# Optimization experiments

Hardware: AMD Instinct MI355X
Metric: run time of the kernel (lower is better)

## Reference

```python
import jax, jax.numpy as jnp
import numpy as np
from jax import lax

N, C1, C2, H, W = 4, 256, 256, 80, 80
CH = 128           # c_ = int(c2 * e)
G, KS = 1, 3       # groups, kernel_size
K = KS * KS        # sampling points per group
PAD, DIL = 1, 1
EPS_BN, EPS_LN = 1e-5, 1e-6


def conv_bn_silu(x, w, g, b, m, v, stride=1):
    # ultralytics Conv: conv(bias=False) + BatchNorm2d(eval) + SiLU
    pad = (w.shape[2] - 1) // 2
    y = lax.conv_general_dilated(x, w, (stride, stride), [(pad, pad), (pad, pad)],
                                 dimension_numbers=('NCHW', 'OIHW', 'NCHW'))
    s = g / jnp.sqrt(v + EPS_BN)
    y = y * s[None, :, None, None] + (b - m * s)[None, :, None, None]
    return jax.nn.silu(y)


def dcnv3_core(x, offset, mask):
    # x: (N,H,W,C) NHWC; offset: (N,H,W,G*K*2); mask: (N,H,W,G,K) softmaxed over K
    n, h, w, c = x.shape
    gc = c // G
    xp = jnp.pad(x, ((0, 0), (PAD, PAD), (PAD, PAD), (0, 0)))
    Hp, Wp = h + 2 * PAD, w + 2 * PAD
    base = (DIL * (KS - 1)) // 2
    # reference points (normalized by padded spatial size), stride 1
    ref_x = (jnp.arange(w, dtype=x.dtype) + base + 0.5) / Wp   # (W,)
    ref_y = (jnp.arange(h, dtype=x.dtype) + base + 0.5) / Hp   # (H,)
    gx = (jnp.arange(KS, dtype=x.dtype) * DIL - base) / Wp
    gy = (jnp.arange(KS, dtype=x.dtype) * DIL - base) / Hp
    grid_x = jnp.repeat(gx, KS)   # point p = i*KS + j -> x = gx[i]
    grid_y = jnp.tile(gy, KS)     # y = gy[j]  (torch meshgrid 'ij' ordering)
    off = offset.reshape(n, h, w, G, K, 2)
    loc_x = ref_x[None, None, :, None, None] + grid_x + off[..., 0] / Wp
    loc_y = ref_y[None, :, None, None, None] + grid_y + off[..., 1] / Hp
    # grid_sample align_corners=False: pixel = norm * size - 0.5
    px = loc_x * Wp - 0.5
    py = loc_y * Hp - 0.5
    x0 = jnp.floor(px); y0 = jnp.floor(py)
    lw, lh = px - x0, py - y0
    x0i, y0i = x0.astype(jnp.int32), y0.astype(jnp.int32)
    xv = jnp.transpose(xp.reshape(n, Hp * Wp, G, gc), (0, 2, 1, 3))  # (N,G,S,gc)
    tw = lambda a: jnp.transpose(a, (0, 3, 1, 2, 4))[..., None]      # (N,H,W,G,K)->(N,G,H,W,K,1)

    def gather(yi, xi):
        valid = ((xi >= 0) & (xi < Wp) & (yi >= 0) & (yi < Hp)).astype(x.dtype)
        idx = jnp.clip(yi, 0, Hp - 1) * Wp + jnp.clip(xi, 0, Wp - 1)
        idx = jnp.transpose(idx, (0, 3, 1, 2, 4)).reshape(n, G, h * w * K)
        v = jnp.take_along_axis(xv, idx[..., None], axis=2).reshape(n, G, h, w, K, gc)
        return v * tw(valid)   # zeros padding_mode

    out = (gather(y0i, x0i) * tw((1 - lh) * (1 - lw))
           + gather(y0i, x0i + 1) * tw((1 - lh) * lw)
           + gather(y0i + 1, x0i) * tw(lh * (1 - lw))
           + gather(y0i + 1, x0i + 1) * tw(lh * lw))   # (N,G,H,W,K,gc)
    m = jnp.transpose(mask, (0, 3, 1, 2, 4))[..., None]
    out = (out * m).sum(axis=4)                        # (N,G,H,W,gc)
    return jnp.transpose(out, (0, 2, 3, 1, 4)).reshape(n, h, w, c)


def forward(x, w1, g1, b1, m1, v1, w2, g2, b2, m2, v2,
            dw_w, dw_b, ln_g, ln_b, off_w, off_b, msk_w, msk_b,
            in_w, in_b, out_w, out_b, g3, b3, m3, v3):
    y = conv_bn_silu(x, w1, g1, b1, m1, v1)   # cv1: 3x3 Conv c1->c_
    y = conv_bn_silu(y, w2, g2, b2, m2, v2)   # cv2.conv: 1x1 Conv c_->c2
    t = jnp.transpose(y, (0, 2, 3, 1))        # NHWC
    x_proj = t @ in_w.T + in_b                # input_proj
    # dw_conv: depthwise 3x3 -> LayerNorm (channels_last) -> GELU
    dw = lax.conv_general_dilated(y, dw_w, (1, 1), [(1, 1), (1, 1)],
                                  dimension_numbers=('NCHW', 'OIHW', 'NCHW'),
                                  feature_group_count=C2)
    dw = jnp.transpose(dw, (0, 2, 3, 1)) + dw_b
    mu = dw.mean(-1, keepdims=True)
    var = ((dw - mu) ** 2).mean(-1, keepdims=True)
    dw = (dw - mu) / jnp.sqrt(var + EPS_LN) * ln_g + ln_b
    dw = jax.nn.gelu(dw, approximate=False)
    offset = dw @ off_w.T + off_b                                       # (N,H,W,G*K*2)
    mask = jax.nn.softmax((dw @ msk_w.T + msk_b).reshape(N, H, W, G, K), axis=-1)
    z = dcnv3_core(x_proj, offset, mask)
    z = z @ out_w.T + out_b                   # output_proj
    z = jnp.transpose(z, (0, 3, 1, 2))        # NCHW
    s = g3 / jnp.sqrt(v3 + EPS_BN)
    z = z * s[None, :, None, None] + (b3 - m3 * s)[None, :, None, None]
    z = jax.nn.silu(z)
    return x + z                              # shortcut (c1 == c2)


def setup_inputs():
    key = jax.random.key(0)
    ks = jax.random.split(key, 16)
    r = lambda k, s, sc=0.05: jax.random.normal(k, s, dtype=jnp.float32) * sc
    return {
        'x': jax.random.normal(ks[0], (N, C1, H, W), dtype=jnp.float32),
        'w1': r(ks[1], (CH, C1, 3, 3)),
        'g1': jnp.ones((CH,), jnp.float32), 'b1': jnp.zeros((CH,), jnp.float32),
        'm1': r(ks[2], (CH,), 0.1),
        'v1': jax.random.uniform(ks[3], (CH,), jnp.float32, 0.5, 1.5),
        'w2': r(ks[4], (C2, CH, 1, 1)),
        'g2': jnp.ones((C2,), jnp.float32), 'b2': jnp.zeros((C2,), jnp.float32),
        'm2': r(ks[5], (C2,), 0.1),
        'v2': jax.random.uniform(ks[6], (C2,), jnp.float32, 0.5, 1.5),
        'dw_w': r(ks[7], (C2, 1, 3, 3)), 'dw_b': jnp.zeros((C2,), jnp.float32),
        'ln_g': jnp.ones((C2,), jnp.float32), 'ln_b': jnp.zeros((C2,), jnp.float32),
        'off_w': r(ks[8], (G * K * 2, C2), 0.01), 'off_b': jnp.zeros((G * K * 2,), jnp.float32),
        'msk_w': r(ks[9], (G * K, C2), 0.01), 'msk_b': jnp.zeros((G * K,), jnp.float32),
        'in_w': r(ks[10], (C2, C2)), 'in_b': jnp.zeros((C2,), jnp.float32),
        'out_w': r(ks[11], (C2, C2)), 'out_b': jnp.zeros((C2,), jnp.float32),
        'g3': jnp.ones((C2,), jnp.float32), 'b3': jnp.zeros((C2,), jnp.float32),
        'm3': r(ks[12], (C2,), 0.1),
        'v3': jax.random.uniform(ks[13], (C2,), jnp.float32, 0.5, 1.5),
    }


def reference(x, w1, g1, b1, m1, v1, w2, g2, b2, m2, v2,
              dw_w, dw_b, ln_g, ln_b, off_w, off_b, msk_w, msk_b,
              in_w, in_b, out_w, out_b, g3, b3, m3, v3):
    return forward(x, w1, g1, b1, m1, v1, w2, g2, b2, m2, v2,
                   dw_w, dw_b, ln_g, ln_b, off_w, off_b, msk_w, msk_b,
                   in_w, in_b, out_w, out_b, g3, b3, m3, v3)
```

## Files before the change

### kernel.cpp

```cpp
#include <hip/hip_runtime.h>
#include <cmath>

#define TN 4
#define TC1 256
#define TCH 128
#define TC2 256
#define TH 80
#define TW 80
#define THP 82
#define TWP 84
#define NPIX (TN*TH*TW)

#define OFF_WBF   0
#define OFF_W2B   294912
#define OFF_INWB  327680
#define OFF_OUTWB 393216
#define OFF_DWT   458752
#define OFF_WCAT  461056
#define OFF_WCATB 467968
#define OFF_T1    468128
#define OFF_T2    468512
#define OFF_T3P   469024
#define OFF_XPAD  469504
#define OFF_Y1B   3997696
#define OFF_Y2N   7525888
#define OFF_DWN   469504
#define OFF_RAWN  10802688
#define OFF_ZN    11493888

typedef __attribute__((ext_vector_type(8))) short bf16x8;
typedef __attribute__((ext_vector_type(4))) float f32x4;

__device__ __forceinline__ float siluf(float v) { return v / (1.f + expf(-v)); }
__device__ __forceinline__ short rnbf(float f) {
  unsigned u = __float_as_uint(f);
  unsigned r = (u + 0x7fffu + ((u >> 16) & 1u)) >> 16;
  return (short)r;
}
__device__ __forceinline__ float bf2f(short s) {
  return __uint_as_float(((unsigned)(unsigned short)s) << 16);
}

__global__ __launch_bounds__(256) void k_prep(
    const float* __restrict__ w1, const float* __restrict__ g1, const float* __restrict__ b1,
    const float* __restrict__ m1, const float* __restrict__ v1,
    const float* __restrict__ w2, const float* __restrict__ g2, const float* __restrict__ b2,
    const float* __restrict__ m2, const float* __restrict__ v2,
    const float* __restrict__ dww, const float* __restrict__ offw, const float* __restrict__ offb,
    const float* __restrict__ mskw, const float* __restrict__ mskb,
    const float* __restrict__ inw, const float* __restrict__ outw, const float* __restrict__ outb,
    const float* __restrict__ g3, const float* __restrict__ b3,
    const float* __restrict__ m3, const float* __restrict__ v3,
    float* __restrict__ ws)
{
  int i = blockIdx.x * 256 + threadIdx.x;
  if (i < 294912) {
    int co = i / 2304; int r = i - co * 2304;
    int tap = r >> 8; int ci = r & 255; int ky = tap / 3; int kx = tap - ky * 3;
    float s = g1[co] * __frsqrt_rn(v1[co] + 1e-5f);
    ((short*)(ws + OFF_WBF))[i] = rnbf(w1[((co * TC1 + ci) * 3 + ky) * 3 + kx] * s);
    return;
  }
  i -= 294912;
  if (i < 32768) {
    int co = i >> 7; int ci = i & 127;
    float s = g2[co] * __frsqrt_rn(v2[co] + 1e-5f);
    ((short*)(ws + OFF_W2B))[i] = rnbf(w2[co * TCH + ci] * s);
    return;
  }
  i -= 32768;
  if (i < 65536) {
    int co = i >> 8; int ci = i & 255;
    ((short*)(ws + OFF_INWB))[i] = rnbf(inw[co * TC2 + ci]);
    return;
  }
  i -= 65536;
  if (i < 65536) {
    int co = i >> 8; int ci = i & 255;
    float s = g3[co] * __frsqrt_rn(v3[co] + 1e-5f);
    ((short*)(ws + OFF_OUTWB))[i] = rnbf(outw[co * TC2 + ci] * s);
    return;
  }
  i -= 65536;
  if (i < 2304) { int c = i & 255; int j = i >> 8; ws[OFF_DWT + i] = dww[c * 9 + j]; return; }
  i -= 2304;
  if (i < 8192) {
    int c = i & 255; int j = i >> 8;
    float v = 0.f;
    if (j < 18) v = offw[j * 256 + c];
    else if (j < 27) v = mskw[(j - 18) * 256 + c];
    ((short*)(ws + OFF_WCAT))[i] = rnbf(v);
    return;
  }
  i -= 8192;
  if (i < 27) { ws[OFF_WCATB + i] = (i < 18) ? offb[i] : mskb[i - 18]; return; }
  i -= 27;
  if (i < 128) { float s = g1[i] / sqrtf(v1[i] + 1e-5f); ws[OFF_T1 + i] = b1[i] - m1[i] * s; return; }
  i -= 128;
  if (i < 256) { float s = g2[i] / sqrtf(v2[i] + 1e-5f); ws[OFF_T2 + i] = b2[i] - m2[i] * s; return; }
  i -= 256;
  if (i < 256) { float s = g3[i] / sqrtf(v3[i] + 1e-5f); ws[OFF_T3P + i] = outb[i] * s + b3[i] - m3[i] * s; return; }
}

__global__ __launch_bounds__(256) void k_padx(const float* __restrict__ x, short* __restrict__ xpn)
{
  __shared__ short lds[80 * 40];
  int b = blockIdx.x;
  int cc = b & 7; int hp = (b >> 3) % THP; int n = b / (THP * 8);
  int c0 = cc * 32;
  int t = threadIdx.x;
  int h = hp - 1;
  bool hv = (h >= 0 && h < TH);
  if (hv) {
    for (int f = t; f < 640; f += 256) {
      int ci = f / 20; int w4 = (f - ci * 20) * 4;
      float4 xv = *(const float4*)(x + ((n * TC1 + c0 + ci) * TH + h) * TW + w4);
      lds[(w4 + 0) * 40 + ci] = rnbf(xv.x);
      lds[(w4 + 1) * 40 + ci] = rnbf(xv.y);
      lds[(w4 + 2) * 40 + ci] = rnbf(xv.z);
      lds[(w4 + 3) * 40 + ci] = rnbf(xv.w);
    }
  }
  __syncthreads();
  short* op = xpn + ((n * THP + hp) * TWP) * TC2 + c0;
  for (int g = t; g < 672; g += 256) {
    int ci4 = (g & 7) * 4; int wp = g >> 3;
    short4 v = {0, 0, 0, 0};
    if (hv && wp >= 1 && wp <= TW) v = *(const short4*)(&lds[(wp - 1) * 40 + ci4]);
    *(short4*)(op + wp * TC2 + ci4) = v;
  }
}

#define BH_STR 40
#define BH_PIX 108
__global__ __launch_bounds__(256) void k_cv1f(const short* __restrict__ xpn, const short* __restrict__ wbf,
                                              const float* __restrict__ t1v, short* __restrict__ y1b)
{
  __shared__ short Bh[2][BH_PIX * BH_STR];

  int b = blockIdx.x;
  int wt = b % 5; b /= 5; int ht = b % 20; int n = b / 20;
  int w0 = wt * 16, h0 = ht * 4;

  int tid = threadIdx.x;
  int wave = tid >> 6, lane = tid & 63;
  int ln = lane & 15, q = lane >> 4;
  int co0 = wave * 32;

  int u0 = tid, u1 = tid + 256;
  int p0 = u0 >> 2, s0 = u0 & 3;
  int p1 = u1 >> 2, s1 = u1 & 3;
  int hh0 = p0 / 18, ww0 = p0 - hh0 * 18;
  int hh1 = p1 / 18, ww1 = p1 - hh1 * 18;
  const short* sb0 = xpn + ((n * THP + h0 + hh0) * TWP + (w0 + ww0)) * 256 + s0 * 8;
  const short* sb1 = xpn + ((n * THP + h0 + hh1) * TWP + (w0 + ww1)) * 256 + s1 * 8;
  bool hasu1 = (u1 < 432);
  int d0 = p0 * BH_STR + s0 * 8;
  int d1 = p1 * BH_STR + s1 * 8;

  const short* abase = wbf + (co0 + ln) * 2304 + q * 8;

  f32x4 acc[2][4];
#pragma unroll
  for (int i = 0; i < 2; ++i)
#pragma unroll
    for (int j = 0; j < 4; ++j) acc[i][j] = (f32x4){0.f, 0.f, 0.f, 0.f};

  bf16x8 rb0 = *(const bf16x8*)(sb0);
  bf16x8 rb1 = {0, 0, 0, 0, 0, 0, 0, 0};
  if (hasu1) rb1 = *(const bf16x8*)(sb1);
  *(bf16x8*)(&Bh[0][d0]) = rb0;
  if (hasu1) *(bf16x8*)(&Bh[0][d1]) = rb1;
  __syncthreads();

  for (int cc = 0; cc < 8; ++cc) {
    int cur = cc & 1;
    bf16x8 af[9][2];
#pragma unroll
    for (int tap = 0; tap < 9; ++tap)
#pragma unroll
      for (int mt = 0; mt < 2; ++mt)
        af[tap][mt] = *(const bf16x8*)(abase + (mt * 16) * 2304 + tap * 256 + cc * 32);
    if (cc < 7) {
      rb0 = *(const bf16x8*)(sb0 + (cc + 1) * 32);
      if (hasu1) rb1 = *(const bf16x8*)(sb1 + (cc + 1) * 32);
    }
#pragma unroll
    for (int tap = 0; tap < 9; ++tap) {
      const int ky = tap / 3, kx = tap - (tap / 3) * 3;
      bf16x8 bv[4];
#pragma unroll
      for (int nt = 0; nt < 4; ++nt) {
        int pr = nt * 16 + ln;
        int hr = pr >> 4, wc = pr & 15;
        bv[nt] = *(const bf16x8*)(&Bh[cur][((hr + ky) * 18 + (wc + kx)) * BH_STR + q * 8]);
      }
#pragma unroll
      for (int mt = 0; mt < 2; ++mt)
#pragma unroll
        for (int nt = 0; nt < 4; ++nt)
          acc[mt][nt] = __builtin_amdgcn_mfma_f32_16x16x32_bf16(af[tap][mt], bv[nt], acc[mt][nt], 0, 0, 0);
    }
    if (cc < 7) {
      *(bf16x8*)(&Bh[cur ^ 1][d0]) = rb0;
      if (hasu1) *(bf16x8*)(&Bh[cur ^ 1][d1]) = rb1;
      __syncthreads();
    }
  }

#pragma unroll
  for (int mt = 0; mt < 2; ++mt) {
    int co = co0 + mt * 16 + q * 4;
    float t0 = t1v[co], t1 = t1v[co + 1], t2 = t1v[co + 2], t3 = t1v[co + 3];
#pragma unroll
    for (int nt = 0; nt < 4; ++nt) {
      int pr = nt * 16 + ln;
      int hr = pr >> 4, wc = pr & 15;
      int pix = (n * TH + h0 + hr) * TW + (w0 + wc);
      short4 p;
      p.x = rnbf(siluf(acc[mt][nt][0] + t0));
      p.y = rnbf(siluf(acc[mt][nt][1] + t1));
      p.z = rnbf(siluf(acc[mt][nt][2] + t2));
      p.w = rnbf(siluf(acc[mt][nt][3] + t3));
      *(short4*)(y1b + pix * TCH + co) = p;
    }
  }
}

#define A_STR 40
__global__ __launch_bounds__(256) void k_cv2(const short* __restrict__ y1b, const short* __restrict__ w2b,
                                             const float* __restrict__ t2v, short* __restrict__ y2b)
{
  __shared__ short As[2][128 * A_STR];
  __shared__ short Bs[2][128 * A_STR];

  int b = blockIdx.x;
  int ch = b & 1; int pt = b >> 1;
  int co_base = ch * 128;
  int pix0 = pt * 128;

  int tid = threadIdx.x;
  int wave = tid >> 6, lane = tid & 63;
  int ln = lane & 15, q = lane >> 4;
  int coh = (wave & 1) * 64;
  int pxh = (wave >> 1) * 64;

  int srow = tid >> 1;
  int ssub = (tid & 1) * 16;
  const short* arow = w2b + (co_base + srow) * TCH + ssub;
  const short* brow = y1b + (pix0 + srow) * TCH + ssub;

  f32x4 acc[4][4];
#pragma unroll
  for (int i = 0; i < 4; ++i)
#pragma unroll
    for (int j = 0; j < 4; ++j) acc[i][j] = (f32x4){0.f, 0.f, 0.f, 0.f};

  bf16x8 ra0, ra1, rb0, rb1;
  auto grab = [&](int c) {
    const short* ap = arow + c * 32;
    const short* bp = brow + c * 32;
    ra0 = *(const bf16x8*)(ap);
    ra1 = *(const bf16x8*)(ap + 8);
    rb0 = *(const bf16x8*)(bp);
    rb1 = *(const bf16x8*)(bp + 8);
  };
  auto put = [&](int buf) {
    int o = srow * A_STR + ssub;
    *(bf16x8*)(&As[buf][o])     = ra0;
    *(bf16x8*)(&As[buf][o + 8]) = ra1;
    *(bf16x8*)(&Bs[buf][o])     = rb0;
    *(bf16x8*)(&Bs[buf][o + 8]) = rb1;
  };
  auto comp = [&](int buf) {
    bf16x8 af[4], bfv[4];
#pragma unroll
    for (int mt = 0; mt < 4; ++mt)
      af[mt] = *(const bf16x8*)(&As[buf][(coh + mt * 16 + ln) * A_STR + q * 8]);
#pragma unroll
    for (int nt = 0; nt < 4; ++nt)
      bfv[nt] = *(const bf16x8*)(&Bs[buf][(pxh + nt * 16 + ln) * A_STR + q * 8]);
#pragma unroll
    for (int mt = 0; mt < 4; ++mt)
#pragma unroll
      for (int nt = 0; nt < 4; ++nt)
        acc[mt][nt] = __builtin_amdgcn_mfma_f32_16x16x32_bf16(af[mt], bfv[nt], acc[mt][nt], 0, 0, 0);
  };

  const int NCH = TCH / 32;
  grab(0);
  put(0);
  __syncthreads();
  for (int c = 0; c < NCH; ++c) {
    if (c < NCH - 1) grab(c + 1);
    comp(c & 1);
    if (c < NCH - 1) {
      __syncthreads();
      put((c + 1) & 1);
      __syncthreads();
    }
  }

#pragma unroll
  for (int mt = 0; mt < 4; ++mt) {
    int co = co_base + coh + mt * 16 + q * 4;
    float t0 = t2v[co], t1 = t2v[co + 1], t2 = t2v[co + 2], t3 = t2v[co + 3];
#pragma unroll
    for (int nt = 0; nt < 4; ++nt) {
      int pix = pix0 + pxh + nt * 16 + ln;
      short4 p;
      p.x = rnbf(siluf(acc[mt][nt][0] + t0));
      p.y = rnbf(siluf(acc[mt][nt][1] + t1));
      p.z = rnbf(siluf(acc[mt][nt][2] + t2));
      p.w = rnbf(siluf(acc[mt][nt][3] + t3));
      *(short4*)(y2b + pix * TC2 + co) = p;
    }
  }
}

__global__ __launch_bounds__(256) void k_proj_in(const short* __restrict__ y2b, const short* __restrict__ inwb,
                                                 const float* __restrict__ inb, short* __restrict__ xproj)
{
  __shared__ short As[2][128 * A_STR];
  __shared__ short Bs[2][128 * A_STR];

  int b = blockIdx.x;
  int ch = b & 1; int pt = b >> 1;
  int co_base = ch * 128;
  int pix0 = pt * 128;

  int tid = threadIdx.x;
  int wave = tid >> 6, lane = tid & 63;
  int ln = lane & 15, q = lane >> 4;
  int coh = (wave & 1) * 64;
  int pxh = (wave >> 1) * 64;

  int srow = tid >> 1;
  int ssub = (tid & 1) * 16;
  const short* arow = inwb + (co_base + srow) * TC2 + ssub;
  const short* brow = y2b + (pix0 + srow) * TC2 + ssub;

  f32x4 acc[4][4];
#pragma unroll
  for (int i = 0; i < 4; ++i)
#pragma unroll
    for (int j = 0; j < 4; ++j) acc[i][j] = (f32x4){0.f, 0.f, 0.f, 0.f};

  bf16x8 ra0, ra1, rb0, rb1;
  auto grab = [&](int c) {
    const short* ap = arow + c * 32;
    const short* bp = brow + c * 32;
    ra0 = *(const bf16x8*)(ap);
    ra1 = *(const bf16x8*)(ap + 8);
    rb0 = *(const bf16x8*)(bp);
    rb1 = *(const bf16x8*)(bp + 8);
  };
  auto put = [&](int buf) {
    int o = srow * A_STR + ssub;
    *(bf16x8*)(&As[buf][o])     = ra0;
    *(bf16x8*)(&As[buf][o + 8]) = ra1;
    *(bf16x8*)(&Bs[buf][o])     = rb0;
    *(bf16x8*)(&Bs[buf][o + 8]) = rb1;
  };
  auto comp = [&](int buf) {
    bf16x8 af[4], bfv[4];
#pragma unroll
    for (int mt = 0; mt < 4; ++mt)
      af[mt] = *(const bf16x8*)(&As[buf][(coh + mt * 16 + ln) * A_STR + q * 8]);
#pragma unroll
    for (int nt = 0; nt < 4; ++nt)
      bfv[nt] = *(const bf16x8*)(&Bs[buf][(pxh + nt * 16 + ln) * A_STR + q * 8]);
#pragma unroll
    for (int mt = 0; mt < 4; ++mt)
#pragma unroll
      for (int nt = 0; nt < 4; ++nt)
        acc[mt][nt] = __builtin_amdgcn_mfma_f32_16x16x32_bf16(af[mt], bfv[nt], acc[mt][nt], 0, 0, 0);
  };

  const int NCH = TC2 / 32;
  grab(0);
  put(0);
  __syncthreads();
  for (int c = 0; c < NCH; ++c) {
    if (c < NCH - 1) grab(c + 1);
    comp(c & 1);
    if (c < NCH - 1) {
      __syncthreads();
      put((c + 1) & 1);
      __syncthreads();
    }
  }

#pragma unroll
  for (int mt = 0; mt < 4; ++mt) {
    int co = co_base + coh + mt * 16 + q * 4;
    float b0 = inb[co], b1 = inb[co + 1], b2 = inb[co + 2], b3 = inb[co + 3];
#pragma unroll
    for (int nt = 0; nt < 4; ++nt) {
      int pix = pix0 + pxh + nt * 16 + ln;
      short4 p;
      p.x = rnbf(acc[mt][nt][0] + b0);
      p.y = rnbf(acc[mt][nt][1] + b1);
      p.z = rnbf(acc[mt][nt][2] + b2);
      p.w = rnbf(acc[mt][nt][3] + b3);
      *(short4*)(xproj + pix * TC2 + co) = p;
    }
  }
}

__global__ __launch_bounds__(256) void k_dwln(const short* __restrict__ y2b, const float* __restrict__ dwt,
                                              const float* __restrict__ dwb, const float* __restrict__ lng,
                                              const float* __restrict__ lnb, short* __restrict__ dwo)
{
  int tid = threadIdx.x;
  int wave = tid >> 6, lane = tid & 63;
  int half = lane >> 5;
  int pix = blockIdx.x * 8 + wave * 2 + half;
  int w = pix % TW; int h = (pix / TW) % TH; int n = pix / (TH * TW);
  int c0 = (lane & 31) * 8;

  float v[8];
  {
    float4 b0 = *(const float4*)(dwb + c0);
    float4 b1 = *(const float4*)(dwb + c0 + 4);
    v[0] = b0.x; v[1] = b0.y; v[2] = b0.z; v[3] = b0.w;
    v[4] = b1.x; v[5] = b1.y; v[6] = b1.z; v[7] = b1.w;
  }
#pragma unroll
  for (int dy = 0; dy < 3; ++dy) {
#pragma unroll
    for (int dx = 0; dx < 3; ++dx) {
      int hh = h + dy - 1, ww = w + dx - 1;
      bool ok = (hh >= 0) & (hh < TH) & (ww >= 0) & (ww < TW);
      int off = ok ? (((n * TH + hh) * TW + ww) * TC2 + c0) : c0;
      bf16x8 yv = *(const bf16x8*)(y2b + off);
      float m = ok ? 1.f : 0.f;
      const float* wp = dwt + (dy * 3 + dx) * TC2 + c0;
      float4 w0 = *(const float4*)(wp);
      float4 w1 = *(const float4*)(wp + 4);
      v[0] += bf2f(yv[0]) * w0.x * m;
      v[1] += bf2f(yv[1]) * w0.y * m;
      v[2] += bf2f(yv[2]) * w0.z * m;
      v[3] += bf2f(yv[3]) * w0.w * m;
      v[4] += bf2f(yv[4]) * w1.x * m;
      v[5] += bf2f(yv[5]) * w1.y * m;
      v[6] += bf2f(yv[6]) * w1.z * m;
      v[7] += bf2f(yv[7]) * w1.w * m;
    }
  }
  float sv = 0.f, sq = 0.f;
#pragma unroll
  for (int i = 0; i < 8; ++i) { sv += v[i]; sq += v[i] * v[i]; }
#pragma unroll
  for (int o = 16; o > 0; o >>= 1) { sv += __shfl_xor(sv, o); sq += __shfl_xor(sq, o); }
  float mu = sv * (1.f / 256.f);
  float var = sq * (1.f / 256.f) - mu * mu;
  float rs = 1.f / sqrtf(var + 1e-6f);
  float4 g0 = *(const float4*)(lng + c0);
  float4 g1 = *(const float4*)(lng + c0 + 4);
  float4 bb0 = *(const float4*)(lnb + c0);
  float4 bb1 = *(const float4*)(lnb + c0 + 4);
  float gv[8] = {g0.x, g0.y, g0.z, g0.w, g1.x, g1.y, g1.z, g1.w};
  float bv[8] = {bb0.x, bb0.y, bb0.z, bb0.w, bb1.x, bb1.y, bb1.z, bb1.w};
  const float is2 = 0.70710678118654752f;
  bf16x8 o8;
#pragma unroll
  for (int i = 0; i < 8; ++i) {
    float nv = (v[i] - mu) * rs * gv[i] + bv[i];
    o8[i] = rnbf(0.5f * nv * (1.f + erff(nv * is2)));
  }
  *(bf16x8*)(dwo + pix * TC2 + c0) = o8;
}

__global__ __launch_bounds__(256) void k_offmask(const short* __restrict__ dwo, const short* __restrict__ wcatb16,
                                                 const float* __restrict__ wcatb, float* __restrict__ raw)
{
  int tid = threadIdx.x;
  int wave = tid >> 6, lane = tid & 63;
  int ln = lane & 15, q = lane >> 4;
  int pix0 = blockIdx.x * 64 + wave * 16;

  f32x4 acc0 = {0.f, 0.f, 0.f, 0.f};
  f32x4 acc1 = acc0;

  const short* a0p = wcatb16 + ln * 256 + q * 8;
  const short* a1p = wcatb16 + (16 + ln) * 256 + q * 8;
  const short* bp  = dwo + (pix0 + ln) * 256 + q * 8;
#pragma unroll
  for (int kk = 0; kk < 256; kk += 32) {
    bf16x8 bf = *(const bf16x8*)(bp + kk);
    bf16x8 a0 = *(const bf16x8*)(a0p + kk);
    bf16x8 a1 = *(const bf16x8*)(a1p + kk);
    acc0 = __builtin_amdgcn_mfma_f32_16x16x32_bf16(a0, bf, acc0, 0, 0, 0);
    acc1 = __builtin_amdgcn_mfma_f32_16x16x32_bf16(a1, bf, acc1, 0, 0, 0);
  }

  int pix = pix0 + ln;
#pragma unroll
  for (int r = 0; r < 4; ++r) {
    int j0 = q * 4 + r;
    raw[pix * 27 + j0] = acc0[r] + wcatb[j0];
    int j1 = 16 + j0;
    if (j1 < 27) raw[pix * 27 + j1] = acc1[r] + wcatb[j1];
  }
}

__global__ __launch_bounds__(256) void k_dcn(const short* __restrict__ xproj, const float* __restrict__ raw,
                                             short* __restrict__ z)
{
  __shared__ int2 sp[8][36];
  int tid = threadIdx.x;
  int pixbase = blockIdx.x * 8;

  for (int j = tid; j < 288; j += 256) {
    int pxl = j / 36, t = j - pxl * 36;
    int pix = pixbase + pxl;
    int w = pix % TW; int h = (pix / TW) % TH;
    const float* r = raw + pix * 27;
    int k = t >> 2, tap = t & 3;
    int tx = tap & 1, ty = tap >> 1;
    float mx = r[18];
#pragma unroll
    for (int kk = 1; kk < 9; ++kk) mx = fmaxf(mx, r[18 + kk]);
    float sum = 0.f, ek = 0.f;
#pragma unroll
    for (int kk = 0; kk < 9; ++kk) {
      float ee = expf(r[18 + kk] - mx);
      sum += ee;
      if (kk == k) ek = ee;
    }
    float mk = ek / sum;
    float px = (float)(w + k / 3) + r[2 * k];
    float py = (float)(h + k % 3) + r[2 * k + 1];
    float x0f = floorf(px), y0f = floorf(py);
    float lw = px - x0f, lh = py - y0f;
    int x0 = (int)x0f + tx, y0 = (int)y0f + ty;
    float wt = mk * (tx ? lw : 1.f - lw) * (ty ? lh : 1.f - lh);
    bool valid = (x0 >= 1) & (x0 <= TW) & (y0 >= 1) & (y0 <= TH);
    int2 pr;
    pr.x = valid ? (((y0 - 1) * TW + (x0 - 1)) * TC2) : 0;
    pr.y = valid ? __float_as_int(wt) : 0;
    sp[pxl][t] = pr;
  }
  __syncthreads();

  int wave = tid >> 6, lane = tid & 63;
  int half = lane >> 5;
  int pxl = wave * 2 + half;
  int pix = pixbase + pxl;
  int n = pix / (TH * TW);
  int c0 = (lane & 31) * 8;
  const short* xb = xproj + n * (TH * TW * TC2) + c0;

  float a[8] = {0.f, 0.f, 0.f, 0.f, 0.f, 0.f, 0.f, 0.f};
#pragma unroll
  for (int t = 0; t < 36; ++t) {
    int2 pr = sp[pxl][t];
    float wt = __int_as_float(pr.y);
    bf16x8 v = *(const bf16x8*)(xb + pr.x);
#pragma unroll
    for (int i = 0; i < 8; ++i) a[i] += wt * bf2f(v[i]);
  }
  bf16x8 o8;
#pragma unroll
  for (int i = 0; i < 8; ++i) o8[i] = rnbf(a[i]);
  *(bf16x8*)(z + pix * TC2 + c0) = o8;
}

__global__ __launch_bounds__(256) void k_proj_out(const short* __restrict__ zb, const short* __restrict__ outwb,
                                                  const float* __restrict__ t3p,
                                                  const float* __restrict__ x, float* __restrict__ out)
{
  __shared__ short As[2][128 * A_STR];
  __shared__ short Bs[2][128 * A_STR];

  int b = blockIdx.x;
  int ch = b & 1; int pt = b >> 1;
  int co_base = ch * 128;
  int pix0 = pt * 128;

  int tid = threadIdx.x;
  int wave = tid >> 6, lane = tid & 63;
  int ln = lane & 15, q = lane >> 4;
  int coh = (wave & 1) * 64;
  int pxh = (wave >> 1) * 64;

  int srow = tid >> 1;
  int ssub = (tid & 1) * 16;
  const short* arow = outwb + (co_base + srow) * TC2 + ssub;
  const short* brow = zb + (pix0 + srow) * TC2 + ssub;

  f32x4 acc[4][4];
#pragma unroll
  for (int i = 0; i < 4; ++i)
#pragma unroll
    for (int j = 0; j < 4; ++j) acc[i][j] = (f32x4){0.f, 0.f, 0.f, 0.f};

  bf16x8 ra0, ra1, rb0, rb1;
  auto grab = [&](int c) {
    const short* ap = arow + c * 32;
    const short* bp = brow + c * 32;
    ra0 = *(const bf16x8*)(ap);
    ra1 = *(const bf16x8*)(ap + 8);
    rb0 = *(const bf16x8*)(bp);
    rb1 = *(const bf16x8*)(bp + 8);
  };
  auto put = [&](int buf) {
    int o = srow * A_STR + ssub;
    *(bf16x8*)(&As[buf][o])     = ra0;
    *(bf16x8*)(&As[buf][o + 8]) = ra1;
    *(bf16x8*)(&Bs[buf][o])     = rb0;
    *(bf16x8*)(&Bs[buf][o + 8]) = rb1;
  };
  auto comp = [&](int buf) {
    bf16x8 af[4], bfv[4];
#pragma unroll
    for (int mt = 0; mt < 4; ++mt)
      af[mt] = *(const bf16x8*)(&As[buf][(coh + mt * 16 + ln) * A_STR + q * 8]);
#pragma unroll
    for (int nt = 0; nt < 4; ++nt)
      bfv[nt] = *(const bf16x8*)(&Bs[buf][(pxh + nt * 16 + ln) * A_STR + q * 8]);
#pragma unroll
    for (int mt = 0; mt < 4; ++mt)
#pragma unroll
      for (int nt = 0; nt < 4; ++nt)
        acc[mt][nt] = __builtin_amdgcn_mfma_f32_16x16x32_bf16(af[mt], bfv[nt], acc[mt][nt], 0, 0, 0);
  };

  const int NCH = TC2 / 32;
  grab(0);
  put(0);
  __syncthreads();
  for (int c = 0; c < NCH; ++c) {
    if (c < NCH - 1) grab(c + 1);
    comp(c & 1);
    if (c < NCH - 1) {
      __syncthreads();
      put((c + 1) & 1);
      __syncthreads();
    }
  }

  __syncthreads();
  float* tb = (float*)(&As[0][0]);
  float* wb = tb + wave * 1056;
  int pixw = pix0 + pxh;
  int nn = pixw / (TH * TW);
  int hw0 = pixw - nn * (TH * TW);

#pragma unroll
  for (int mt = 0; mt < 4; ++mt) {
#pragma unroll
    for (int nt = 0; nt < 4; ++nt)
#pragma unroll
      for (int r = 0; r < 4; ++r)
        wb[(q * 4 + r) * 66 + nt * 16 + ln] = acc[mt][nt][r];
    int co = co_base + coh + mt * 16;
#pragma unroll
    for (int cl = 0; cl < 16; ++cl) {
      float vv = wb[cl * 66 + lane];
      int addr = (nn * TC2 + co + cl) * (TH * TW) + hw0 + lane;
      out[addr] = x[addr] + siluf(vv + t3p[co + cl]);
    }
  }
}

extern "C" void kernel_launch(void* const* d_in, const int* in_sizes, int n_in,
                              void* d_out, int out_size, void* d_ws, size_t ws_size,
                              hipStream_t stream)
{
  const float* x    = (const float*)d_in[0];
  const float* w1   = (const float*)d_in[1];
  const float* g1   = (const float*)d_in[2];
  const float* b1   = (const float*)d_in[3];
  const float* m1   = (const float*)d_in[4];
  const float* v1   = (const float*)d_in[5];
  const float* w2   = (const float*)d_in[6];
  const float* g2   = (const float*)d_in[7];
  const float* b2   = (const float*)d_in[8];
  const float* m2   = (const float*)d_in[9];
  const float* v2   = (const float*)d_in[10];
  const float* dww  = (const float*)d_in[11];
  const float* dwb  = (const float*)d_in[12];
  const float* lng  = (const float*)d_in[13];
  const float* lnb  = (const float*)d_in[14];
  const float* offw = (const float*)d_in[15];
  const float* offb = (const float*)d_in[16];
  const float* mskw = (const float*)d_in[17];
  const float* mskb = (const float*)d_in[18];
  const float* inw  = (const float*)d_in[19];
  const float* inb  = (const float*)d_in[20];
  const float* outw = (const float*)d_in[21];
  const float* outb = (const float*)d_in[22];
  const float* g3   = (const float*)d_in[23];
  const float* b3   = (const float*)d_in[24];
  const float* m3   = (const float*)d_in[25];
  const float* v3   = (const float*)d_in[26];

  float* ws  = (float*)d_ws;
  float* out = (float*)d_out;

  short* xpn    = (short*)(ws + OFF_XPAD);
  short* wbf    = (short*)(ws + OFF_WBF);
  short* w2b    = (short*)(ws + OFF_W2B);
  short* inwb   = (short*)(ws + OFF_INWB);
  short* outwb  = (short*)(ws + OFF_OUTWB);
  short* wcat16 = (short*)(ws + OFF_WCAT);
  short* y1b    = (short*)(ws + OFF_Y1B);
  short* y2b    = (short*)(ws + OFF_Y2N);
  short* dwo    = (short*)(ws + OFF_DWN);
  float* raw    = ws + OFF_RAWN;
  short* zb     = (short*)(ws + OFF_ZN);
  short* xproj  = (short*)d_out;

  hipLaunchKernelGGL(k_prep, dim3(1836), dim3(256), 0, stream,
                     w1, g1, b1, m1, v1, w2, g2, b2, m2, v2,
                     dww, offw, offb, mskw, mskb, inw, outw, outb, g3, b3, m3, v3, ws);
  hipLaunchKernelGGL(k_padx,     dim3(TN * THP * 8), dim3(256), 0, stream, x, xpn);
  hipLaunchKernelGGL(k_cv1f,     dim3(400),   dim3(256), 0, stream, xpn, wbf, ws + OFF_T1, y1b);
  hipLaunchKernelGGL(k_cv2,      dim3(400),   dim3(256), 0, stream, y1b, w2b, ws + OFF_T2, y2b);
  hipLaunchKernelGGL(k_proj_in,  dim3(400),   dim3(256), 0, stream, y2b, inwb, inb, xproj);
  hipLaunchKernelGGL(k_dwln,     dim3(3200),  dim3(256), 0, stream, y2b, ws + OFF_DWT, dwb, lng, lnb, dwo);
  hipLaunchKernelGGL(k_offmask,  dim3(400),   dim3(256), 0, stream, dwo, wcat16, ws + OFF_WCATB, raw);
  hipLaunchKernelGGL(k_dcn,      dim3(3200),  dim3(256), 0, stream, xproj, raw, zb);
  hipLaunchKernelGGL(k_proj_out, dim3(400),   dim3(256), 0, stream, zb, outwb, ws + OFF_T3P, x, out);
}
```

Before: 275.5 us.

## Load full input halo tile into LDS once instead of double-buffered channel chunks

```diff
diff --git a/kernel.cpp b/kernel.cpp
--- a/kernel.cpp
+++ b/kernel.cpp
@@ -131,12 +131,12 @@
   }
 }
 
-#define BH_STR 40
-#define BH_PIX 108
+#define FH_STR 264
+#define FH_PIX 108
 __global__ __launch_bounds__(256) void k_cv1f(const short* __restrict__ xpn, const short* __restrict__ wbf,
                                               const float* __restrict__ t1v, short* __restrict__ y1b)
 {
-  __shared__ short Bh[2][BH_PIX * BH_STR];
+  __shared__ short Bh[FH_PIX * FH_STR];
 
   int b = blockIdx.x;
   int wt = b % 5; b /= 5; int ht = b % 20; int n = b / 20;
@@ -147,16 +147,13 @@
   int ln = lane & 15, q = lane >> 4;
   int co0 = wave * 32;
 
-  int u0 = tid, u1 = tid + 256;
-  int p0 = u0 >> 2, s0 = u0 & 3;
-  int p1 = u1 >> 2, s1 = u1 & 3;
-  int hh0 = p0 / 18, ww0 = p0 - hh0 * 18;
-  int hh1 = p1 / 18, ww1 = p1 - hh1 * 18;
-  const short* sb0 = xpn + ((n * THP + h0 + hh0) * TWP + (w0 + ww0)) * 256 + s0 * 8;
-  const short* sb1 = xpn + ((n * THP + h0 + hh1) * TWP + (w0 + ww1)) * 256 + s1 * 8;
-  bool hasu1 = (u1 < 432);
-  int d0 = p0 * BH_STR + s0 * 8;
-  int d1 = p1 * BH_STR + s1 * 8;
+  for (int g = tid; g < FH_PIX * 32; g += 256) {
+    int px = g >> 5, s = g & 31;
+    int hh = px / 18, ww = px - hh * 18;
+    bf16x8 v = *(const bf16x8*)(xpn + ((n * THP + h0 + hh) * TWP + (w0 + ww)) * 256 + s * 8);
+    *(bf16x8*)(&Bh[px * FH_STR + s * 8]) = v;
+  }
+  __syncthreads();
 
   const short* abase = wbf + (co0 + ln) * 2304 + q * 8;
 
@@ -166,45 +163,25 @@
 #pragma unroll
     for (int j = 0; j < 4; ++j) acc[i][j] = (f32x4){0.f, 0.f, 0.f, 0.f};
 
-  bf16x8 rb0 = *(const bf16x8*)(sb0);
-  bf16x8 rb1 = {0, 0, 0, 0, 0, 0, 0, 0};
-  if (hasu1) rb1 = *(const bf16x8*)(sb1);
-  *(bf16x8*)(&Bh[0][d0]) = rb0;
-  if (hasu1) *(bf16x8*)(&Bh[0][d1]) = rb1;
-  __syncthreads();
-
   for (int cc = 0; cc < 8; ++cc) {
-    int cur = cc & 1;
     bf16x8 af[9][2];
 #pragma unroll
     for (int tap = 0; tap < 9; ++tap)
 #pragma unroll
       for (int mt = 0; mt < 2; ++mt)
         af[tap][mt] = *(const bf16x8*)(abase + (mt * 16) * 2304 + tap * 256 + cc * 32);
-    if (cc < 7) {
-      rb0 = *(const bf16x8*)(sb0 + (cc + 1) * 32);
-      if (hasu1) rb1 = *(const bf16x8*)(sb1 + (cc + 1) * 32);
-    }
 #pragma unroll
     for (int tap = 0; tap < 9; ++tap) {
       const int ky = tap / 3, kx = tap - (tap / 3) * 3;
       bf16x8 bv[4];
 #pragma unroll
-      for (int nt = 0; nt < 4; ++nt) {
-        int pr = nt * 16 + ln;
-        int hr = pr >> 4, wc = pr & 15;
-        bv[nt] = *(const bf16x8*)(&Bh[cur][((hr + ky) * 18 + (wc + kx)) * BH_STR + q * 8]);
-      }
+      for (int nt = 0; nt < 4; ++nt)
+        bv[nt] = *(const bf16x8*)(&Bh[((nt + ky) * 18 + (ln + kx)) * FH_STR + cc * 32 + q * 8]);
 #pragma unroll
       for (int mt = 0; mt < 2; ++mt)
 #pragma unroll
         for (int nt = 0; nt < 4; ++nt)
           acc[mt][nt] = __builtin_amdgcn_mfma_f32_16x16x32_bf16(af[tap][mt], bv[nt], acc[mt][nt], 0, 0, 0);
-    }
-    if (cc < 7) {
-      *(bf16x8*)(&Bh[cur ^ 1][d0]) = rb0;
-      if (hasu1) *(bf16x8*)(&Bh[cur ^ 1][d1]) = rb1;
-      __syncthreads();
     }
   }
 
@@ -214,9 +191,7 @@
     float t0 = t1v[co], t1 = t1v[co + 1], t2 = t1v[co + 2], t3 = t1v[co + 3];
 #pragma unroll
     for (int nt = 0; nt < 4; ++nt) {
-      int pr = nt * 16 + ln;
-      int hr = pr >> 4, wc = pr & 15;
-      int pix = (n * TH + h0 + hr) * TW + (w0 + wc);
+      int pix = (n * TH + h0 + nt) * TW + (w0 + ln);
       short4 p;
       p.x = rnbf(siluf(acc[mt][nt][0] + t0));
       p.y = rnbf(siluf(acc[mt][nt][1] + t1));
```

Measured after the change: 273.3 us. About the same (-0.8%).

## Fuse depthwise conv+LayerNorm+GELU with offset/mask projection via shared memory

Applied to the files above, without the earlier changes.

```diff
diff --git a/kernel.cpp b/kernel.cpp
--- a/kernel.cpp
+++ b/kernel.cpp
@@ -24,7 +24,6 @@
 #define OFF_XPAD  469504
 #define OFF_Y1B   3997696
 #define OFF_Y2N   7525888
-#define OFF_DWN   469504
 #define OFF_RAWN  10802688
 #define OFF_ZN    11493888
 
@@ -408,100 +407,96 @@
   }
 }
 
-__global__ __launch_bounds__(256) void k_dwln(const short* __restrict__ y2b, const float* __restrict__ dwt,
+#define DT_STR 264
+__global__ __launch_bounds__(256) void k_dwom(const short* __restrict__ y2b, const float* __restrict__ dwt,
                                               const float* __restrict__ dwb, const float* __restrict__ lng,
-                                              const float* __restrict__ lnb, short* __restrict__ dwo)
-{
+                                              const float* __restrict__ lnb,
+                                              const short* __restrict__ wcatb16,
+                                              const float* __restrict__ wcatb,
+                                              float* __restrict__ raw)
+{
+  __shared__ short dt[32 * DT_STR];
+
   int tid = threadIdx.x;
   int wave = tid >> 6, lane = tid & 63;
   int half = lane >> 5;
-  int pix = blockIdx.x * 8 + wave * 2 + half;
-  int w = pix % TW; int h = (pix / TW) % TH; int n = pix / (TH * TW);
   int c0 = (lane & 31) * 8;
-
-  float v[8];
-  {
-    float4 b0 = *(const float4*)(dwb + c0);
-    float4 b1 = *(const float4*)(dwb + c0 + 4);
-    v[0] = b0.x; v[1] = b0.y; v[2] = b0.z; v[3] = b0.w;
-    v[4] = b1.x; v[5] = b1.y; v[6] = b1.z; v[7] = b1.w;
-  }
-#pragma unroll
-  for (int dy = 0; dy < 3; ++dy) {
-#pragma unroll
-    for (int dx = 0; dx < 3; ++dx) {
-      int hh = h + dy - 1, ww = w + dx - 1;
-      bool ok = (hh >= 0) & (hh < TH) & (ww >= 0) & (ww < TW);
-      int off = ok ? (((n * TH + hh) * TW + ww) * TC2 + c0) : c0;
-      bf16x8 yv = *(const bf16x8*)(y2b + off);
-      float m = ok ? 1.f : 0.f;
-      const float* wp = dwt + (dy * 3 + dx) * TC2 + c0;
-      float4 w0 = *(const float4*)(wp);
-      float4 w1 = *(const float4*)(wp + 4);
-      v[0] += bf2f(yv[0]) * w0.x * m;
-      v[1] += bf2f(yv[1]) * w0.y * m;
-      v[2] += bf2f(yv[2]) * w0.z * m;
-      v[3] += bf2f(yv[3]) * w0.w * m;
-      v[4] += bf2f(yv[4]) * w1.x * m;
-      v[5] += bf2f(yv[5]) * w1.y * m;
-      v[6] += bf2f(yv[6]) * w1.z * m;
-      v[7] += bf2f(yv[7]) * w1.w * m;
-    }
-  }
-  float sv = 0.f, sq = 0.f;
-#pragma unroll
-  for (int i = 0; i < 8; ++i) { sv += v[i]; sq += v[i] * v[i]; }
-#pragma unroll
-  for (int o = 16; o > 0; o >>= 1) { sv += __shfl_xor(sv, o); sq += __shfl_xor(sq, o); }
-  float mu = sv * (1.f / 256.f);
-  float var = sq * (1.f / 256.f) - mu * mu;
-  float rs = 1.f / sqrtf(var + 1e-6f);
+  int pix0 = blockIdx.x * 32;
+
+  float4 db0 = *(const float4*)(dwb + c0);
+  float4 db1 = *(const float4*)(dwb + c0 + 4);
   float4 g0 = *(const float4*)(lng + c0);
   float4 g1 = *(const float4*)(lng + c0 + 4);
-  float4 bb0 = *(const float4*)(lnb + c0);
-  float4 bb1 = *(const float4*)(lnb + c0 + 4);
+  float4 lb0 = *(const float4*)(lnb + c0);
+  float4 lb1 = *(const float4*)(lnb + c0 + 4);
   float gv[8] = {g0.x, g0.y, g0.z, g0.w, g1.x, g1.y, g1.z, g1.w};
-  float bv[8] = {bb0.x, bb0.y, bb0.z, bb0.w, bb1.x, bb1.y, bb1.z, bb1.w};
+  float bv[8] = {lb0.x, lb0.y, lb0.z, lb0.w, lb1.x, lb1.y, lb1.z, lb1.w};
   const float is2 = 0.70710678118654752f;
-  bf16x8 o8;
-#pragma unroll
-  for (int i = 0; i < 8; ++i) {
-    float nv = (v[i] - mu) * rs * gv[i] + bv[i];
-    o8[i] = rnbf(0.5f * nv * (1.f + erff(nv * is2)));
-  }
-  *(bf16x8*)(dwo + pix * TC2 + c0) = o8;
-}
-
-__global__ __launch_bounds__(256) void k_offmask(const short* __restrict__ dwo, const short* __restrict__ wcatb16,
-                                                 const float* __restrict__ wcatb, float* __restrict__ raw)
-{
-  int tid = threadIdx.x;
-  int wave = tid >> 6, lane = tid & 63;
+
+  for (int r = 0; r < 4; ++r) {
+    int pl = wave * 8 + half * 4 + r;
+    int pix = pix0 + pl;
+    int w = pix % TW; int h = (pix / TW) % TH; int n = pix / (TH * TW);
+    float v[8] = {db0.x, db0.y, db0.z, db0.w, db1.x, db1.y, db1.z, db1.w};
+#pragma unroll
+    for (int dy = 0; dy < 3; ++dy) {
+#pragma unroll
+      for (int dx = 0; dx < 3; ++dx) {
+        int hh = h + dy - 1, ww = w + dx - 1;
+        bool ok = (hh >= 0) & (hh < TH) & (ww >= 0) & (ww < TW);
+        int off = ok ? (((n * TH + hh) * TW + ww) * TC2 + c0) : c0;
+        bf16x8 yv = *(const bf16x8*)(y2b + off);
+        float m = ok ? 1.f : 0.f;
+        const float* wp = dwt + (dy * 3 + dx) * TC2 + c0;
+        float4 w0 = *(const float4*)(wp);
+        float4 w1 = *(const float4*)(wp + 4);
+        v[0] += bf2f(yv[0]) * w0.x * m;
+        v[1] += bf2f(yv[1]) * w0.y * m;
+        v[2] += bf2f(yv[2]) * w0.z * m;
+        v[3] += bf2f(yv[3]) * w0.w * m;
+        v[4] += bf2f(yv[4]) * w1.x * m;
+        v[5] += bf2f(yv[5]) * w1.y * m;
+        v[6] += bf2f(yv[6]) * w1.z * m;
+        v[7] += bf2f(yv[7]) * w1.w * m;
+      }
+    }
+    float sv = 0.f, sq = 0.f;
+#pragma unroll
+    for (int i = 0; i < 8; ++i) { sv += v[i]; sq += v[i] * v[i]; }
+#pragma unroll
+    for (int o = 16; o > 0; o >>= 1) { sv += __shfl_xor(sv, o); sq += __shfl_xor(sq, o); }
+    float mu = sv * (1.f / 256.f);
+    float var = sq * (1.f / 256.f) - mu * mu;
+    float rs = 1.f / sqrtf(var + 1e-6f);
+    bf16x8 o8;
+#pragma unroll
+    for (int i = 0; i < 8; ++i) {
+      float nv = (v[i] - mu) * rs * gv[i] + bv[i];
+      o8[i] = rnbf(0.5f * nv * (1.f + erff(nv * is2)));
+    }
+    *(bf16x8*)(&dt[pl * DT_STR + c0]) = o8;
+  }
+  __syncthreads();
+
   int ln = lane & 15, q = lane >> 4;
-  int pix0 = blockIdx.x * 64 + wave * 16;
-
-  f32x4 acc0 = {0.f, 0.f, 0.f, 0.f};
-  f32x4 acc1 = acc0;
-
-  const short* a0p = wcatb16 + ln * 256 + q * 8;
-  const short* a1p = wcatb16 + (16 + ln) * 256 + q * 8;
-  const short* bp  = dwo + (pix0 + ln) * 256 + q * 8;
+  int g = wave & 1;
+  int jbase = (wave >> 1) * 16;
+
+  f32x4 acc = {0.f, 0.f, 0.f, 0.f};
+  const short* ap = wcatb16 + (jbase + ln) * 256 + q * 8;
+  const short* bp = &dt[(g * 16 + ln) * DT_STR + q * 8];
 #pragma unroll
   for (int kk = 0; kk < 256; kk += 32) {
+    bf16x8 a  = *(const bf16x8*)(ap + kk);
     bf16x8 bf = *(const bf16x8*)(bp + kk);
-    bf16x8 a0 = *(const bf16x8*)(a0p + kk);
-    bf16x8 a1 = *(const bf16x8*)(a1p + kk);
-    acc0 = __builtin_amdgcn_mfma_f32_16x16x32_bf16(a0, bf, acc0, 0, 0, 0);
-    acc1 = __builtin_amdgcn_mfma_f32_16x16x32_bf16(a1, bf, acc1, 0, 0, 0);
-  }
-
-  int pix = pix0 + ln;
+    acc = __builtin_amdgcn_mfma_f32_16x16x32_bf16(a, bf, acc, 0, 0, 0);
+  }
+
+  int pix = pix0 + g * 16 + ln;
 #pragma unroll
   for (int r = 0; r < 4; ++r) {
-    int j0 = q * 4 + r;
-    raw[pix * 27 + j0] = acc0[r] + wcatb[j0];
-    int j1 = 16 + j0;
-    if (j1 < 27) raw[pix * 27 + j1] = acc1[r] + wcatb[j1];
+    int j = jbase + q * 4 + r;
+    if (j < 27) raw[pix * 27 + j] = acc[r] + wcatb[j];
   }
 }
 
@@ -708,7 +703,6 @@
   short* wcat16 = (short*)(ws + OFF_WCAT);
   short* y1b    = (short*)(ws + OFF_Y1B);
   short* y2b    = (short*)(ws + OFF_Y2N);
-  short* dwo    = (short*)(ws + OFF_DWN);
   float* raw    = ws + OFF_RAWN;
   short* zb     = (short*)(ws + OFF_ZN);
   short* xproj  = (short*)d_out;
@@ -720,8 +714,8 @@
   hipLaunchKernelGGL(k_cv1f,     dim3(400),   dim3(256), 0, stream, xpn, wbf, ws + OFF_T1, y1b);
   hipLaunchKernelGGL(k_cv2,      dim3(400),   dim3(256), 0, stream, y1b, w2b, ws + OFF_T2, y2b);
   hipLaunchKernelGGL(k_proj_in,  dim3(400),   dim3(256), 0, stream, y2b, inwb, inb, xproj);
-  hipLaunchKernelGGL(k_dwln,     dim3(3200),  dim3(256), 0, stream, y2b, ws + OFF_DWT, dwb, lng, lnb, dwo);
-  hipLaunchKernelGGL(k_offmask,  dim3(400),   dim3(256), 0, stream, dwo, wcat16, ws + OFF_WCATB, raw);
+  hipLaunchKernelGGL(k_dwom,     dim3(800),   dim3(256), 0, stream, y2b, ws + OFF_DWT, dwb, lng, lnb,
+                     wcat16, ws + OFF_WCATB, raw);
   hipLaunchKernelGGL(k_dcn,      dim3(3200),  dim3(256), 0, stream, xproj, raw, zb);
   hipLaunchKernelGGL(k_proj_out, dim3(400),   dim3(256), 0, stream, zb, outwb, ws + OFF_T3P, x, out);
 }
```

Measured after the change: 276.3 us. About the same (+0.3%).
